# Optimization experiments

Measured on AMD Instinct MI355X. Metric: run time of the kernel, lower is better.

The kernel has to match this reference:

```python
import jax, jax.numpy as jnp
import numpy as np

D_MODEL = 2048
N_HEADS = 16
HEAD_DIM = D_MODEL // N_HEADS
D_FF = 4 * D_MODEL
B, L = 2, 2048
EPS = 1e-5


def _layernorm(x, g, b):
    mu = jnp.mean(x, axis=-1, keepdims=True)
    var = jnp.var(x, axis=-1, keepdims=True)
    return (x - mu) * jax.lax.rsqrt(var + EPS) * g + b


def setup_inputs() -> dict:
    key = jax.random.key(0)
    ks = jax.random.split(key, 8)
    s = 0.02
    x = jax.random.normal(ks[0], (B, L, D_MODEL), dtype=jnp.float32)
    # causal 4-D float mask [B,1,L,L]: 1 = attend, 0 = masked
    attention_mask = jnp.broadcast_to(
        jnp.tril(jnp.ones((L, L), dtype=jnp.float32))[None, None], (B, 1, L, L)
    )
    w_qkv = jax.random.normal(ks[1], (D_MODEL, 3 * D_MODEL), dtype=jnp.float32) * s
    w_o = jax.random.normal(ks[2], (D_MODEL, D_MODEL), dtype=jnp.float32) * s
    w1 = jax.random.normal(ks[3], (D_MODEL, D_FF), dtype=jnp.float32) * s
    b1 = jnp.zeros((D_FF,), dtype=jnp.float32)
    w2 = jax.random.normal(ks[4], (D_FF, D_MODEL), dtype=jnp.float32) * s
    b2 = jnp.zeros((D_MODEL,), dtype=jnp.float32)
    g_ln1 = jnp.ones((D_MODEL,), dtype=jnp.float32)
    b_ln1 = jnp.zeros((D_MODEL,), dtype=jnp.float32)
    g_ln2 = jnp.ones((D_MODEL,), dtype=jnp.float32)
    b_ln2 = jnp.zeros((D_MODEL,), dtype=jnp.float32)
    return {
        "x": x, "attention_mask": attention_mask,
        "w_qkv": w_qkv, "w_o": w_o,
        "g_ln1": g_ln1, "b_ln1": b_ln1, "g_ln2": g_ln2, "b_ln2": b_ln2,
        "w1": w1, "b1": b1, "w2": w2, "b2": b2,
    }


def reference(x, attention_mask, w_qkv, w_o, g_ln1, b_ln1, g_ln2, b_ln2, w1, b1, w2, b2):
    Bx, Lx, D = x.shape
    residual = x
    h = _layernorm(x, g_ln1, b_ln1)
    qkv = (h @ w_qkv).reshape(Bx, Lx, 3, N_HEADS, HEAD_DIM)
    q, k, v = jnp.moveaxis(qkv, 2, 0)           # each [B, L, H, Hd]
    q = q.transpose(0, 2, 1, 3)                  # [B, H, L, Hd]
    k = k.transpose(0, 2, 1, 3)
    v = v.transpose(0, 2, 1, 3)
    scores = jnp.einsum("bhqd,bhkd->bhqk", q, k) / np.float32(np.sqrt(HEAD_DIM))
    scores = scores + (1.0 - attention_mask) * -10000.0  # 4-D float mask branch
    attn = jax.nn.softmax(scores, axis=-1)
    out = jnp.einsum("bhqk,bhkd->bhqd", attn, v)
    out = out.transpose(0, 2, 1, 3).reshape(Bx, Lx, D)
    out = out @ w_o
    x2 = residual + out
    h2 = _layernorm(x2, g_ln2, b_ln2)
    mlp = jax.nn.gelu(h2 @ w1 + b1, approximate=False) @ w2 + b2
    return x2 + mlp
```

## Files before the change

### kernel.cpp

```cpp
#include <hip/hip_runtime.h>
#include <hip/hip_bf16.h>

#define DM   2048
#define LSEQ 2048
#define NB   2
#define NH   16
#define HDIM 128
#define DFF  8192

typedef __attribute__((ext_vector_type(8))) short bf16x8;
typedef __attribute__((ext_vector_type(4))) float f32x4;

typedef __attribute__((address_space(1))) void gvoid;
typedef __attribute__((address_space(3))) void lvoid;
#define GLDS16(g, s) __builtin_amdgcn_global_load_lds((const gvoid*)(g), (lvoid*)(s), 16, 0, 0)

__device__ __forceinline__ unsigned short f2b(float f) {
    __hip_bfloat16 h = __float2bfloat16(f);
    return *reinterpret_cast<unsigned short*>(&h);
}

__global__ __launch_bounds__(256) void transpose_bf16(const float* __restrict__ in,
                                                      unsigned short* __restrict__ out,
                                                      int R, int C) {
    __shared__ float t[32][33];
    const int c0 = blockIdx.x * 32, r0 = blockIdx.y * 32;
    const int tx = threadIdx.x, ty = threadIdx.y;
#pragma unroll
    for (int i = 0; i < 4; i++)
        t[ty + 8 * i][tx] = in[(size_t)(r0 + ty + 8 * i) * C + c0 + tx];
    __syncthreads();
#pragma unroll
    for (int i = 0; i < 4; i++)
        out[(size_t)(c0 + ty + 8 * i) * R + r0 + tx] = f2b(t[tx][ty + 8 * i]);
}

__global__ __launch_bounds__(256) void ln_k(const float* __restrict__ x,
                                            const float* __restrict__ g,
                                            const float* __restrict__ bta,
                                            unsigned short* __restrict__ out) {
    const int row = blockIdx.x, tid = threadIdx.x;
    const float* xr = x + (size_t)row * DM;
    float4 v0 = *(const float4*)&xr[tid * 4];
    float4 v1 = *(const float4*)&xr[1024 + tid * 4];
    float s  = v0.x + v0.y + v0.z + v0.w + v1.x + v1.y + v1.z + v1.w;
    float ss = v0.x * v0.x + v0.y * v0.y + v0.z * v0.z + v0.w * v0.w
             + v1.x * v1.x + v1.y * v1.y + v1.z * v1.z + v1.w * v1.w;
#pragma unroll
    for (int o = 32; o; o >>= 1) { s += __shfl_down(s, o); ss += __shfl_down(ss, o); }
    __shared__ float red[8];
    const int w = tid >> 6, l = tid & 63;
    if (l == 0) { red[w] = s; red[4 + w] = ss; }
    __syncthreads();
    s  = red[0] + red[1] + red[2] + red[3];
    ss = red[4] + red[5] + red[6] + red[7];
    const float mu  = s * (1.0f / DM);
    const float var = ss * (1.0f / DM) - mu * mu;
    const float rst = rsqrtf(var + 1e-5f);
    float4 g0 = *(const float4*)&g[tid * 4];
    float4 b0 = *(const float4*)&bta[tid * 4];
    float4 g1 = *(const float4*)&g[1024 + tid * 4];
    float4 b1 = *(const float4*)&bta[1024 + tid * 4];
    ushort4 o0, o1;
    o0.x = f2b((v0.x - mu) * rst * g0.x + b0.x);
    o0.y = f2b((v0.y - mu) * rst * g0.y + b0.y);
    o0.z = f2b((v0.z - mu) * rst * g0.z + b0.z);
    o0.w = f2b((v0.w - mu) * rst * g0.w + b0.w);
    o1.x = f2b((v1.x - mu) * rst * g1.x + b1.x);
    o1.y = f2b((v1.y - mu) * rst * g1.y + b1.y);
    o1.z = f2b((v1.z - mu) * rst * g1.z + b1.z);
    o1.w = f2b((v1.w - mu) * rst * g1.w + b1.w);
    *(ushort4*)&out[(size_t)row * DM + tid * 4] = o0;
    *(ushort4*)&out[(size_t)row * DM + 1024 + tid * 4] = o1;
}

template <bool BIAS, bool GELU_, bool RES, bool OUTBF>
__global__ __launch_bounds__(256) void gemm_k(const unsigned short* __restrict__ A,
                                              const unsigned short* __restrict__ Bt,
                                              const float* __restrict__ bias,
                                              const float* __restrict__ res,
                                              void* __restrict__ outp,
                                              int M, int N, int K) {
    __shared__ unsigned short Al[128 * 32];
    __shared__ unsigned short Bl[128 * 32];
    const int tid = threadIdx.x, w = tid >> 6, l = tid & 63;
    const int n0 = blockIdx.x * 128, m0 = blockIdx.y * 128;
    const int wr = (w >> 1) * 64, wc = (w & 1) * 64;
    const int lr = l & 15, ko = (l >> 4) * 8;
    f32x4 acc[4][4] = {};

    const int srow = w * 32 + (l >> 2);
    const int skk  = (l & 3) * 8;
    const unsigned short* ga0 = A + (size_t)(m0 + srow) * K + skk;
    const unsigned short* ga1 = ga0 + (size_t)16 * K;
    const unsigned short* gb0 = Bt + (size_t)(n0 + srow) * K + skk;
    const unsigned short* gb1 = gb0 + (size_t)16 * K;
    unsigned short* la = &Al[w * 1024];
    unsigned short* lb = &Bl[w * 1024];
    const int nk = K >> 5;
    for (int kt = 0; kt < nk; ++kt) {
        GLDS16(ga0, la);
        GLDS16(ga1, la + 512);
        GLDS16(gb0, lb);
        GLDS16(gb1, lb + 512);
        ga0 += 32; ga1 += 32; gb0 += 32; gb1 += 32;
        __syncthreads();
        bf16x8 af[4], bv[4];
#pragma unroll
        for (int i = 0; i < 4; i++) af[i] = *(const bf16x8*)&Al[(wr + i * 16 + lr) * 32 + ko];
#pragma unroll
        for (int i = 0; i < 4; i++) bv[i] = *(const bf16x8*)&Bl[(wc + i * 16 + lr) * 32 + ko];
#pragma unroll
        for (int i = 0; i < 4; i++)
#pragma unroll
            for (int j = 0; j < 4; j++)
                acc[i][j] = __builtin_amdgcn_mfma_f32_16x16x32_bf16(af[i], bv[j], acc[i][j], 0, 0, 0);
        __syncthreads();
    }
#pragma unroll
    for (int j = 0; j < 4; j++) {
        const int col = n0 + wc + j * 16 + lr;
        const float bvv = BIAS ? bias[col] : 0.0f;
#pragma unroll
        for (int i = 0; i < 4; i++) {
#pragma unroll
            for (int r = 0; r < 4; r++) {
                const int row = m0 + wr + i * 16 + (l >> 4) * 4 + r;
                float v = acc[i][j][r] + bvv;
                if (GELU_) v = 0.5f * v * (1.0f + erff(v * 0.7071067811865476f));
                if (RES) v += res[(size_t)row * N + col];
                if (OUTBF) ((unsigned short*)outp)[(size_t)row * N + col] = f2b(v);
                else       ((float*)outp)[(size_t)row * N + col] = v;
            }
        }
    }
}

__global__ __launch_bounds__(256) void flash_attn_k(const unsigned short* __restrict__ qkv,
                                                    unsigned short* __restrict__ out) {
    __shared__ unsigned short Kl[64 * 136];
    __shared__ unsigned short Vt[128 * 64];
    __shared__ unsigned short Pl[4][16 * 72];
    const int tid = threadIdx.x, w = tid >> 6, l = tid & 63;
    const int bh = blockIdx.y, b = bh >> 4, h = bh & 15;
    const int lr = l & 15, lg = l >> 4;
    const float sc = 0.08838834764831845f;
    const int NT = LSEQ / 64;

#pragma unroll 1
    for (int pi = 0; pi < 2; ++pi) {
        const int qt = (pi == 0) ? (int)blockIdx.x : (NT - 1 - (int)blockIdx.x);
        const int qw = qt * 64 + w * 16;

        bf16x8 qf[4];
        {
            const unsigned short* qb = qkv + (size_t)(b * LSEQ + qw + lr) * (3 * DM) + h * HDIM + lg * 8;
#pragma unroll
            for (int kc = 0; kc < 4; kc++) qf[kc] = *(const bf16x8*)(qb + kc * 32);
        }
        f32x4 O[8] = {};
        float m_run[4] = {-1e30f, -1e30f, -1e30f, -1e30f};
        float l_run[4] = {};

        for (int kt = 0; kt <= qt; ++kt) {
            const int k0 = kt * 64;
#pragma unroll
            for (int i = 0; i < 4; i++) {
                const int seg = i * 256 + tid;
                const int row = seg >> 4;
                const int c8  = (seg & 15) * 8;
                const unsigned short* src = qkv + (size_t)(b * LSEQ + k0 + row) * (3 * DM) + DM + h * HDIM + c8;
                *(uint4*)&Kl[row * 136 + c8] = *(const uint4*)src;
                unsigned short tmp[8];
                *(uint4*)tmp = *(const uint4*)(src + DM);
#pragma unroll
                for (int j = 0; j < 8; j++) {
                    const int d = c8 + j;
                    Vt[d * 64 + (row ^ ((((d >> 3) ^ d) & 7) << 3))] = tmp[j];
                }
            }
            __syncthreads();
            f32x4 S[4] = {};
#pragma unroll
            for (int st = 0; st < 4; ++st)
#pragma unroll
                for (int kc = 0; kc < 4; kc++) {
                    bf16x8 kb = *(const bf16x8*)&Kl[(st * 16 + lr) * 136 + kc * 32 + lg * 8];
                    S[st] = __builtin_amdgcn_mfma_f32_16x16x32_bf16(qf[kc], kb, S[st], 0, 0, 0);
                }
            const bool last = (kt == qt);
#pragma unroll
            for (int r = 0; r < 4; r++) {
                const int row = qw + lg * 4 + r;
                float s0 = S[0][r] * sc, s1 = S[1][r] * sc, s2 = S[2][r] * sc, s3 = S[3][r] * sc;
                if (last) {
                    if (k0 +  0 + lr > row) s0 = -1e30f;
                    if (k0 + 16 + lr > row) s1 = -1e30f;
                    if (k0 + 32 + lr > row) s2 = -1e30f;
                    if (k0 + 48 + lr > row) s3 = -1e30f;
                }
                float mt = fmaxf(fmaxf(s0, s1), fmaxf(s2, s3));
                mt = fmaxf(mt, __shfl_xor(mt, 1));
                mt = fmaxf(mt, __shfl_xor(mt, 2));
                mt = fmaxf(mt, __shfl_xor(mt, 4));
                mt = fmaxf(mt, __shfl_xor(mt, 8));
                const float mn = fmaxf(m_run[r], mt);
                const float al = __expf(m_run[r] - mn);
                m_run[r] = mn;
                float p0 = __expf(s0 - mn), p1 = __expf(s1 - mn), p2 = __expf(s2 - mn), p3 = __expf(s3 - mn);
                float ts = p0 + p1 + p2 + p3;
                ts += __shfl_xor(ts, 1);
                ts += __shfl_xor(ts, 2);
                ts += __shfl_xor(ts, 4);
                ts += __shfl_xor(ts, 8);
                l_run[r] = l_run[r] * al + ts;
#pragma unroll
                for (int c = 0; c < 8; c++) O[c][r] *= al;
                unsigned short* pr = &Pl[w][(lg * 4 + r) * 72 + lr];
                pr[0] = f2b(p0); pr[16] = f2b(p1); pr[32] = f2b(p2); pr[48] = f2b(p3);
            }
#pragma unroll
            for (int ks = 0; ks < 2; ++ks) {
                bf16x8 pa = *(const bf16x8*)&Pl[w][lr * 72 + ks * 32 + lg * 8];
#pragma unroll
                for (int c = 0; c < 8; c++) {
                    const int d = c * 16 + lr;
                    bf16x8 vb = *(const bf16x8*)&Vt[d * 64 + ((ks * 32 + lg * 8) ^ ((((d >> 3) ^ d) & 7) << 3))];
                    O[c] = __builtin_amdgcn_mfma_f32_16x16x32_bf16(pa, vb, O[c], 0, 0, 0);
                }
            }
            __syncthreads();
        }
#pragma unroll
        for (int r = 0; r < 4; r++) {
            const float inv = 1.0f / l_run[r];
            const size_t ro = (size_t)(b * LSEQ + qw + lg * 4 + r) * DM + h * HDIM;
#pragma unroll
            for (int c = 0; c < 8; c++) out[ro + c * 16 + lr] = f2b(O[c][r] * inv);
        }
    }
}

extern "C" void kernel_launch(void* const* d_in, const int* in_sizes, int n_in,
                              void* d_out, int out_size, void* d_ws, size_t ws_size,
                              hipStream_t stream) {
    const float* x     = (const float*)d_in[0];
    const float* w_qkv = (const float*)d_in[2];
    const float* w_o   = (const float*)d_in[3];
    const float* g1    = (const float*)d_in[4];
    const float* bl1   = (const float*)d_in[5];
    const float* g2    = (const float*)d_in[6];
    const float* bl2   = (const float*)d_in[7];
    const float* w1    = (const float*)d_in[8];
    const float* b1    = (const float*)d_in[9];
    const float* w2    = (const float*)d_in[10];
    const float* b2    = (const float*)d_in[11];
    float* out = (float*)d_out;

    unsigned char* p = (unsigned char*)d_ws;
    unsigned short* wqkvT = (unsigned short*)p; p += (size_t)3 * DM * DM * 2;
    unsigned short* woT   = (unsigned short*)p; p += (size_t)DM * DM * 2;
    unsigned short* w1T   = (unsigned short*)p; p += (size_t)DFF * DM * 2;
    unsigned short* w2T   = (unsigned short*)p; p += (size_t)DM * DFF * 2;
    unsigned short* hbuf  = (unsigned short*)p; p += (size_t)NB * LSEQ * DM * 2;
    unsigned short* big   = (unsigned short*)p; p += (size_t)NB * LSEQ * DFF * 2;
    float* x2 = out;

    const int R = NB * LSEQ;
    dim3 tb(32, 8);
    transpose_bf16<<<dim3(3 * DM / 32, DM / 32), tb, 0, stream>>>(w_qkv, wqkvT, DM, 3 * DM);
    transpose_bf16<<<dim3(DM / 32, DM / 32), tb, 0, stream>>>(w_o, woT, DM, DM);
    transpose_bf16<<<dim3(DFF / 32, DM / 32), tb, 0, stream>>>(w1, w1T, DM, DFF);
    transpose_bf16<<<dim3(DM / 32, DFF / 32), tb, 0, stream>>>(w2, w2T, DFF, DM);

    ln_k<<<R, 256, 0, stream>>>(x, g1, bl1, hbuf);
    gemm_k<false, false, false, true><<<dim3(3 * DM / 128, R / 128), 256, 0, stream>>>(
        hbuf, wqkvT, nullptr, nullptr, big, R, 3 * DM, DM);
    flash_attn_k<<<dim3(LSEQ / 128, NB * NH), 256, 0, stream>>>(big, hbuf);
    gemm_k<false, false, true, false><<<dim3(DM / 128, R / 128), 256, 0, stream>>>(
        hbuf, woT, nullptr, x, x2, R, DM, DM);
    ln_k<<<R, 256, 0, stream>>>(x2, g2, bl2, hbuf);
    gemm_k<true, true, false, true><<<dim3(DFF / 128, R / 128), 256, 0, stream>>>(
        hbuf, w1T, b1, nullptr, big, R, DFF, DM);
    gemm_k<true, false, true, false><<<dim3(DM / 128, R / 128), 256, 0, stream>>>(
        big, w2T, b2, x2, out, R, DM, DFF);
}
```

Measured before the change: 805.9 us.

## Add 256x256 eight-wave pipelined GEMM for QKV and FFN1 projections

```diff
diff --git a/kernel.cpp b/kernel.cpp
--- a/kernel.cpp
+++ b/kernel.cpp
@@ -136,6 +136,158 @@
     }
 }
 
+#define WAITVM4() asm volatile("s_waitcnt vmcnt(4)" ::: "memory")
+#define WAITVM0() asm volatile("s_waitcnt vmcnt(0)" ::: "memory")
+#define WAITLG()  asm volatile("s_waitcnt lgkmcnt(0)" ::: "memory")
+#define MFMA_BEGIN() do { __builtin_amdgcn_s_barrier(); WAITLG(); \
+    __builtin_amdgcn_sched_barrier(0); __builtin_amdgcn_s_setprio(1); } while (0)
+#define MFMA_END() do { __builtin_amdgcn_s_setprio(0); __builtin_amdgcn_s_barrier(); } while (0)
+
+template <int S, int HM>
+__device__ __forceinline__ void read_a(const unsigned short* LDSu, bf16x8 (&af)[8],
+                                       int wr, int lr, int ko) {
+    const unsigned short* pa = LDSu + S * 16384 + wr * 8192;
+#pragma unroll
+    for (int mi = 0; mi < 4; mi++)
+#pragma unroll
+        for (int ks = 0; ks < 2; ks++)
+            af[mi * 2 + ks] = *(const bf16x8*)&pa[ks * 4096 + (HM * 64 + mi * 16 + lr) * 32 + ko];
+}
+template <int S, int HN>
+__device__ __forceinline__ void read_b(const unsigned short* LDSu, bf16x8 (&bf)[4],
+                                       int wc, int lr, int ko) {
+    const unsigned short* pb = LDSu + 32768 + S * 16384 + (wc >> 1) * 8192;
+#pragma unroll
+    for (int nj = 0; nj < 2; nj++)
+#pragma unroll
+        for (int ks = 0; ks < 2; ks++)
+            bf[nj * 2 + ks] = *(const bf16x8*)&pb[ks * 4096 + ((wc & 1) * 64 + HN * 32 + nj * 16 + lr) * 32 + ko];
+}
+template <int HM, int HN>
+__device__ __forceinline__ void quad(f32x4 (&acc)[8][4], const bf16x8 (&af)[8],
+                                     const bf16x8 (&bf)[4]) {
+#pragma unroll
+    for (int mi = 0; mi < 4; mi++)
+#pragma unroll
+        for (int nj = 0; nj < 2; nj++)
+#pragma unroll
+            for (int ks = 0; ks < 2; ks++)
+                acc[HM * 4 + mi][HN * 2 + nj] = __builtin_amdgcn_mfma_f32_16x16x32_bf16(
+                    af[mi * 2 + ks], bf[nj * 2 + ks], acc[HM * 4 + mi][HN * 2 + nj], 0, 0, 0);
+}
+
+template <bool BIAS, bool GELU_>
+__global__ __launch_bounds__(512, 2) void gemm8_k(const unsigned short* __restrict__ A,
+                                                  const unsigned short* __restrict__ Bt,
+                                                  const float* __restrict__ bias,
+                                                  unsigned short* __restrict__ out,
+                                                  int N, int K, int nbx) {
+    extern __shared__ unsigned short LDSu[];
+    const int tid = threadIdx.x, w = tid >> 6, l = tid & 63;
+    const int wr = w >> 2, wc = w & 3;
+    const int lr = l & 15, lg = l >> 4, ko = lg * 8;
+    const int id = blockIdx.x, nwg = gridDim.x;
+    const int swz = (id & 7) * (nwg >> 3) + (id >> 3);
+    const int m0 = (swz / nbx) * 256, n0 = (swz % nbx) * 256;
+
+    const int r = tid >> 2, cc0 = (tid & 3) * 8;
+    const unsigned short* a0row = A + (size_t)(m0 + r) * K + cc0;
+    const unsigned short* a1row = a0row + (size_t)128 * K;
+    const unsigned short* b0row = Bt + (size_t)(n0 + r) * K + cc0;
+    const unsigned short* b1row = b0row + (size_t)128 * K;
+
+#define STAGE_A(S, H, ROW, KOFF) do { \
+    GLDS16((ROW) + (KOFF),      LDSu + (S) * 16384 + (H) * 8192 + tid * 8); \
+    GLDS16((ROW) + (KOFF) + 32, LDSu + (S) * 16384 + (H) * 8192 + 4096 + tid * 8); } while (0)
+#define STAGE_B(S, H, ROW, KOFF) do { \
+    GLDS16((ROW) + (KOFF),      LDSu + 32768 + (S) * 16384 + (H) * 8192 + tid * 8); \
+    GLDS16((ROW) + (KOFF) + 32, LDSu + 32768 + (S) * 16384 + (H) * 8192 + 4096 + tid * 8); } while (0)
+
+    f32x4 acc[8][4] = {};
+    bf16x8 af[8], bf0[4], bf1[4];
+
+    STAGE_A(0, 0, a0row, 0);
+    STAGE_A(0, 1, a1row, 0);
+    STAGE_B(0, 0, b0row, 0);
+    STAGE_B(0, 1, b1row, 0);
+    STAGE_B(1, 0, b0row, 64);
+    STAGE_B(1, 1, b1row, 64);
+    WAITVM4();
+    __builtin_amdgcn_s_barrier();
+
+    const int niter = K >> 7;
+    for (int i = 0; i < niter; ++i) {
+        const bool last = (i == niter - 1);
+        const int k1 = (2 * i + 1) * 64, k2 = k1 + 64, k3 = k1 + 128;
+        read_a<0, 0>(LDSu, af, wr, lr, ko);
+        read_b<0, 0>(LDSu, bf0, wc, lr, ko);
+        STAGE_A(1, 0, a0row, k1);
+        MFMA_BEGIN(); quad<0, 0>(acc, af, bf0); MFMA_END();
+        read_b<0, 1>(LDSu, bf1, wc, lr, ko);
+        STAGE_A(1, 1, a1row, k1);
+        MFMA_BEGIN(); quad<0, 1>(acc, af, bf1); MFMA_END();
+        read_a<0, 1>(LDSu, af, wr, lr, ko);
+        if (!last) STAGE_B(0, 0, b0row, k2);
+        MFMA_BEGIN(); quad<1, 1>(acc, af, bf1); MFMA_END();
+        if (!last) { STAGE_B(0, 1, b1row, k2); WAITVM4(); } else { WAITVM0(); }
+        MFMA_BEGIN(); quad<1, 0>(acc, af, bf0); MFMA_END();
+        read_a<1, 0>(LDSu, af, wr, lr, ko);
+        read_b<1, 0>(LDSu, bf0, wc, lr, ko);
+        if (!last) STAGE_A(0, 0, a0row, k2);
+        MFMA_BEGIN(); quad<0, 0>(acc, af, bf0); MFMA_END();
+        read_b<1, 1>(LDSu, bf1, wc, lr, ko);
+        if (!last) STAGE_A(0, 1, a1row, k2);
+        MFMA_BEGIN(); quad<0, 1>(acc, af, bf1); MFMA_END();
+        read_a<1, 1>(LDSu, af, wr, lr, ko);
+        if (!last) STAGE_B(1, 0, b0row, k3);
+        MFMA_BEGIN(); quad<1, 1>(acc, af, bf1); MFMA_END();
+        if (!last) { STAGE_B(1, 1, b1row, k3); WAITVM4(); }
+        MFMA_BEGIN(); quad<1, 0>(acc, af, bf0); MFMA_END();
+    }
+
+    float* eb = (float*)&LDSu[(size_t)w * 2176];
+    const int row16 = l >> 2, ch = l & 3;
+    float4 bv[4];
+    if (BIAS) {
+#pragma unroll
+        for (int q = 0; q < 4; q++)
+            bv[q] = *(const float4*)&bias[n0 + wc * 64 + ch * 16 + q * 4];
+    }
+#pragma unroll 1
+    for (int mi8 = 0; mi8 < 8; ++mi8) {
+        WAITLG();
+        __builtin_amdgcn_sched_barrier(0);
+#pragma unroll
+        for (int nj = 0; nj < 4; nj++)
+#pragma unroll
+            for (int rr = 0; rr < 4; rr++)
+                eb[(lg * 4 + rr) * 68 + nj * 16 + lr] = acc[mi8][nj][rr];
+        WAITLG();
+        __builtin_amdgcn_sched_barrier(0);
+        alignas(16) unsigned short tmp[16];
+#pragma unroll
+        for (int q = 0; q < 4; q++) {
+            float4 v = *(const float4*)&eb[row16 * 68 + ch * 16 + q * 4];
+            float e0 = v.x, e1 = v.y, e2 = v.z, e3 = v.w;
+            if (BIAS) { e0 += bv[q].x; e1 += bv[q].y; e2 += bv[q].z; e3 += bv[q].w; }
+            if (GELU_) {
+                e0 = 0.5f * e0 * (1.0f + erff(e0 * 0.7071067811865476f));
+                e1 = 0.5f * e1 * (1.0f + erff(e1 * 0.7071067811865476f));
+                e2 = 0.5f * e2 * (1.0f + erff(e2 * 0.7071067811865476f));
+                e3 = 0.5f * e3 * (1.0f + erff(e3 * 0.7071067811865476f));
+            }
+            tmp[q * 4 + 0] = f2b(e0); tmp[q * 4 + 1] = f2b(e1);
+            tmp[q * 4 + 2] = f2b(e2); tmp[q * 4 + 3] = f2b(e3);
+        }
+        unsigned short* dst = out + (size_t)(m0 + wr * 128 + mi8 * 16 + row16) * N
+                              + n0 + wc * 64 + ch * 16;
+        *(uint4*)dst = *(const uint4*)tmp;
+        *(uint4*)(dst + 8) = *(const uint4*)(tmp + 8);
+    }
+#undef STAGE_A
+#undef STAGE_B
+}
+
 __global__ __launch_bounds__(256) void flash_attn_k(const unsigned short* __restrict__ qkv,
                                                     unsigned short* __restrict__ out) {
     __shared__ unsigned short Kl[64 * 136];
@@ -188,12 +340,12 @@
                     bf16x8 kb = *(const bf16x8*)&Kl[(st * 16 + lr) * 136 + kc * 32 + lg * 8];
                     S[st] = __builtin_amdgcn_mfma_f32_16x16x32_bf16(qf[kc], kb, S[st], 0, 0, 0);
                 }
-            const bool last = (kt == qt);
-#pragma unroll
-            for (int r = 0; r < 4; r++) {
-                const int row = qw + lg * 4 + r;
-                float s0 = S[0][r] * sc, s1 = S[1][r] * sc, s2 = S[2][r] * sc, s3 = S[3][r] * sc;
-                if (last) {
+            const bool lastt = (kt == qt);
+#pragma unroll
+            for (int rq = 0; rq < 4; rq++) {
+                const int row = qw + lg * 4 + rq;
+                float s0 = S[0][rq] * sc, s1 = S[1][rq] * sc, s2 = S[2][rq] * sc, s3 = S[3][rq] * sc;
+                if (lastt) {
                     if (k0 +  0 + lr > row) s0 = -1e30f;
                     if (k0 + 16 + lr > row) s1 = -1e30f;
                     if (k0 + 32 + lr > row) s2 = -1e30f;
@@ -204,19 +356,19 @@
                 mt = fmaxf(mt, __shfl_xor(mt, 2));
                 mt = fmaxf(mt, __shfl_xor(mt, 4));
                 mt = fmaxf(mt, __shfl_xor(mt, 8));
-                const float mn = fmaxf(m_run[r], mt);
-                const float al = __expf(m_run[r] - mn);
-                m_run[r] = mn;
+                const float mn = fmaxf(m_run[rq], mt);
+                const float al = __expf(m_run[rq] - mn);
+                m_run[rq] = mn;
                 float p0 = __expf(s0 - mn), p1 = __expf(s1 - mn), p2 = __expf(s2 - mn), p3 = __expf(s3 - mn);
                 float ts = p0 + p1 + p2 + p3;
                 ts += __shfl_xor(ts, 1);
                 ts += __shfl_xor(ts, 2);
                 ts += __shfl_xor(ts, 4);
                 ts += __shfl_xor(ts, 8);
-                l_run[r] = l_run[r] * al + ts;
-#pragma unroll
-                for (int c = 0; c < 8; c++) O[c][r] *= al;
-                unsigned short* pr = &Pl[w][(lg * 4 + r) * 72 + lr];
+                l_run[rq] = l_run[rq] * al + ts;
+#pragma unroll
+                for (int c = 0; c < 8; c++) O[c][rq] *= al;
+                unsigned short* pr = &Pl[w][(lg * 4 + rq) * 72 + lr];
                 pr[0] = f2b(p0); pr[16] = f2b(p1); pr[32] = f2b(p2); pr[48] = f2b(p3);
             }
 #pragma unroll
@@ -232,11 +384,11 @@
             __syncthreads();
         }
 #pragma unroll
-        for (int r = 0; r < 4; r++) {
-            const float inv = 1.0f / l_run[r];
-            const size_t ro = (size_t)(b * LSEQ + qw + lg * 4 + r) * DM + h * HDIM;
-#pragma unroll
-            for (int c = 0; c < 8; c++) out[ro + c * 16 + lr] = f2b(O[c][r] * inv);
+        for (int rq = 0; rq < 4; rq++) {
+            const float inv = 1.0f / l_run[rq];
+            const size_t ro = (size_t)(b * LSEQ + qw + lg * 4 + rq) * DM + h * HDIM;
+#pragma unroll
+            for (int c = 0; c < 8; c++) out[ro + c * 16 + lr] = f2b(O[c][rq] * inv);
         }
     }
 }
@@ -274,14 +426,14 @@
     transpose_bf16<<<dim3(DM / 32, DFF / 32), tb, 0, stream>>>(w2, w2T, DFF, DM);
 
     ln_k<<<R, 256, 0, stream>>>(x, g1, bl1, hbuf);
-    gemm_k<false, false, false, true><<<dim3(3 * DM / 128, R / 128), 256, 0, stream>>>(
-        hbuf, wqkvT, nullptr, nullptr, big, R, 3 * DM, DM);
+    gemm8_k<false, false><<<(R / 256) * (3 * DM / 256), 512, 131072, stream>>>(
+        hbuf, wqkvT, nullptr, big, 3 * DM, DM, 3 * DM / 256);
     flash_attn_k<<<dim3(LSEQ / 128, NB * NH), 256, 0, stream>>>(big, hbuf);
     gemm_k<false, false, true, false><<<dim3(DM / 128, R / 128), 256, 0, stream>>>(
         hbuf, woT, nullptr, x, x2, R, DM, DM);
     ln_k<<<R, 256, 0, stream>>>(x2, g2, bl2, hbuf);
-    gemm_k<true, true, false, true><<<dim3(DFF / 128, R / 128), 256, 0, stream>>>(
-        hbuf, w1T, b1, nullptr, big, R, DFF, DM);
+    gemm8_k<true, true><<<(R / 256) * (DFF / 256), 512, 131072, stream>>>(
+        hbuf, w1T, b1, big, DFF, DM, DFF / 256);
     gemm_k<true, false, true, false><<<dim3(DM / 128, R / 128), 256, 0, stream>>>(
         big, w2T, b2, x2, out, R, DM, DFF);
 }
```

Result: slower. 905.4 us (+12.3%).

## Stage bf16 GEMM epilogue through LDS for vectorized stores and remap block order

Applied to the files above, without the earlier changes.

```diff
diff --git a/kernel.cpp b/kernel.cpp
--- a/kernel.cpp
+++ b/kernel.cpp
@@ -14,6 +14,7 @@
 typedef __attribute__((address_space(1))) void gvoid;
 typedef __attribute__((address_space(3))) void lvoid;
 #define GLDS16(g, s) __builtin_amdgcn_global_load_lds((const gvoid*)(g), (lvoid*)(s), 16, 0, 0)
+#define WAITLG()  asm volatile("s_waitcnt lgkmcnt(0)" ::: "memory")
 
 __device__ __forceinline__ unsigned short f2b(float f) {
     __hip_bfloat16 h = __float2bfloat16(f);
@@ -75,18 +76,23 @@
 }
 
 template <bool BIAS, bool GELU_, bool RES, bool OUTBF>
-__global__ __launch_bounds__(256) void gemm_k(const unsigned short* __restrict__ A,
-                                              const unsigned short* __restrict__ Bt,
-                                              const float* __restrict__ bias,
-                                              const float* __restrict__ res,
-                                              void* __restrict__ outp,
-                                              int M, int N, int K) {
-    __shared__ unsigned short Al[128 * 32];
-    __shared__ unsigned short Bl[128 * 32];
+__global__ __launch_bounds__(256) void gemm2_k(const unsigned short* __restrict__ A,
+                                               const unsigned short* __restrict__ Bt,
+                                               const float* __restrict__ bias,
+                                               const float* __restrict__ res,
+                                               void* __restrict__ outp,
+                                               int M, int N, int K) {
+    __shared__ unsigned short SH[8704];
+    unsigned short* Al = SH;
+    unsigned short* Bl = SH + 4096;
     const int tid = threadIdx.x, w = tid >> 6, l = tid & 63;
-    const int n0 = blockIdx.x * 128, m0 = blockIdx.y * 128;
+    const int flat = blockIdx.y * gridDim.x + blockIdx.x;
+    const int xx = flat & 7, jj = flat >> 3;
+    const int by = 4 * xx + (jj & 3);
+    const int bx = jj >> 2;
+    const int n0 = bx * 128, m0 = by * 128;
     const int wr = (w >> 1) * 64, wc = (w & 1) * 64;
-    const int lr = l & 15, ko = (l >> 4) * 8;
+    const int lr = l & 15, lg = l >> 4, ko = lg * 8;
     f32x4 acc[4][4] = {};
 
     const int srow = w * 32 + (l >> 2);
@@ -117,20 +123,61 @@
                 acc[i][j] = __builtin_amdgcn_mfma_f32_16x16x32_bf16(af[i], bv[j], acc[i][j], 0, 0, 0);
         __syncthreads();
     }
-#pragma unroll
-    for (int j = 0; j < 4; j++) {
-        const int col = n0 + wc + j * 16 + lr;
-        const float bvv = BIAS ? bias[col] : 0.0f;
+    if (OUTBF) {
+        float* eb = (float*)SH + w * 1088;
+        const int row16 = l >> 2, ch = l & 3;
+        float4 bvv[4];
+        if (BIAS) {
+#pragma unroll
+            for (int q = 0; q < 4; q++)
+                bvv[q] = *(const float4*)&bias[n0 + wc + ch * 16 + q * 4];
+        }
 #pragma unroll
         for (int i = 0; i < 4; i++) {
-#pragma unroll
-            for (int r = 0; r < 4; r++) {
-                const int row = m0 + wr + i * 16 + (l >> 4) * 4 + r;
-                float v = acc[i][j][r] + bvv;
-                if (GELU_) v = 0.5f * v * (1.0f + erff(v * 0.7071067811865476f));
-                if (RES) v += res[(size_t)row * N + col];
-                if (OUTBF) ((unsigned short*)outp)[(size_t)row * N + col] = f2b(v);
-                else       ((float*)outp)[(size_t)row * N + col] = v;
+            WAITLG();
+            __builtin_amdgcn_sched_barrier(0);
+#pragma unroll
+            for (int j = 0; j < 4; j++)
+#pragma unroll
+                for (int r = 0; r < 4; r++)
+                    eb[(lg * 4 + r) * 68 + j * 16 + lr] = acc[i][j][r];
+            WAITLG();
+            __builtin_amdgcn_sched_barrier(0);
+            alignas(16) unsigned short tmp[16];
+#pragma unroll
+            for (int q = 0; q < 4; q++) {
+                float4 v = *(const float4*)&eb[row16 * 68 + ch * 16 + q * 4];
+                float e0 = v.x, e1 = v.y, e2 = v.z, e3 = v.w;
+                if (BIAS) { e0 += bvv[q].x; e1 += bvv[q].y; e2 += bvv[q].z; e3 += bvv[q].w; }
+                if (GELU_) {
+                    e0 = 0.5f * e0 * (1.0f + erff(e0 * 0.7071067811865476f));
+                    e1 = 0.5f * e1 * (1.0f + erff(e1 * 0.7071067811865476f));
+                    e2 = 0.5f * e2 * (1.0f + erff(e2 * 0.7071067811865476f));
+                    e3 = 0.5f * e3 * (1.0f + erff(e3 * 0.7071067811865476f));
+                }
+                tmp[q * 4 + 0] = f2b(e0); tmp[q * 4 + 1] = f2b(e1);
+                tmp[q * 4 + 2] = f2b(e2); tmp[q * 4 + 3] = f2b(e3);
+            }
+            unsigned short* dst = (unsigned short*)outp
+                                  + (size_t)(m0 + wr + i * 16 + row16) * N + n0 + wc + ch * 16;
+            *(uint4*)dst = *(const uint4*)tmp;
+            *(uint4*)(dst + 8) = *(const uint4*)(tmp + 8);
+        }
+    } else {
+#pragma unroll
+        for (int j = 0; j < 4; j++) {
+            const int col = n0 + wc + j * 16 + lr;
+            const float bvv = BIAS ? bias[col] : 0.0f;
+#pragma unroll
+            for (int i = 0; i < 4; i++) {
+#pragma unroll
+                for (int r = 0; r < 4; r++) {
+                    const int row = m0 + wr + i * 16 + lg * 4 + r;
+                    float v = acc[i][j][r] + bvv;
+                    if (GELU_) v = 0.5f * v * (1.0f + erff(v * 0.7071067811865476f));
+                    if (RES) v += res[(size_t)row * N + col];
+                    ((float*)outp)[(size_t)row * N + col] = v;
+                }
             }
         }
     }
@@ -188,12 +235,12 @@
                     bf16x8 kb = *(const bf16x8*)&Kl[(st * 16 + lr) * 136 + kc * 32 + lg * 8];
                     S[st] = __builtin_amdgcn_mfma_f32_16x16x32_bf16(qf[kc], kb, S[st], 0, 0, 0);
                 }
-            const bool last = (kt == qt);
-#pragma unroll
-            for (int r = 0; r < 4; r++) {
-                const int row = qw + lg * 4 + r;
-                float s0 = S[0][r] * sc, s1 = S[1][r] * sc, s2 = S[2][r] * sc, s3 = S[3][r] * sc;
-                if (last) {
+            const bool lastt = (kt == qt);
+#pragma unroll
+            for (int rq = 0; rq < 4; rq++) {
+                const int row = qw + lg * 4 + rq;
+                float s0 = S[0][rq] * sc, s1 = S[1][rq] * sc, s2 = S[2][rq] * sc, s3 = S[3][rq] * sc;
+                if (lastt) {
                     if (k0 +  0 + lr > row) s0 = -1e30f;
                     if (k0 + 16 + lr > row) s1 = -1e30f;
                     if (k0 + 32 + lr > row) s2 = -1e30f;
@@ -204,19 +251,19 @@
                 mt = fmaxf(mt, __shfl_xor(mt, 2));
                 mt = fmaxf(mt, __shfl_xor(mt, 4));
                 mt = fmaxf(mt, __shfl_xor(mt, 8));
-                const float mn = fmaxf(m_run[r], mt);
-                const float al = __expf(m_run[r] - mn);
-                m_run[r] = mn;
+                const float mn = fmaxf(m_run[rq], mt);
+                const float al = __expf(m_run[rq] - mn);
+                m_run[rq] = mn;
                 float p0 = __expf(s0 - mn), p1 = __expf(s1 - mn), p2 = __expf(s2 - mn), p3 = __expf(s3 - mn);
                 float ts = p0 + p1 + p2 + p3;
                 ts += __shfl_xor(ts, 1);
                 ts += __shfl_xor(ts, 2);
                 ts += __shfl_xor(ts, 4);
                 ts += __shfl_xor(ts, 8);
-                l_run[r] = l_run[r] * al + ts;
-#pragma unroll
-                for (int c = 0; c < 8; c++) O[c][r] *= al;
-                unsigned short* pr = &Pl[w][(lg * 4 + r) * 72 + lr];
+                l_run[rq] = l_run[rq] * al + ts;
+#pragma unroll
+                for (int c = 0; c < 8; c++) O[c][rq] *= al;
+                unsigned short* pr = &Pl[w][(lg * 4 + rq) * 72 + lr];
                 pr[0] = f2b(p0); pr[16] = f2b(p1); pr[32] = f2b(p2); pr[48] = f2b(p3);
             }
 #pragma unroll
@@ -232,11 +279,11 @@
             __syncthreads();
         }
 #pragma unroll
-        for (int r = 0; r < 4; r++) {
-            const float inv = 1.0f / l_run[r];
-            const size_t ro = (size_t)(b * LSEQ + qw + lg * 4 + r) * DM + h * HDIM;
-#pragma unroll
-            for (int c = 0; c < 8; c++) out[ro + c * 16 + lr] = f2b(O[c][r] * inv);
+        for (int rq = 0; rq < 4; rq++) {
+            const float inv = 1.0f / l_run[rq];
+            const size_t ro = (size_t)(b * LSEQ + qw + lg * 4 + rq) * DM + h * HDIM;
+#pragma unroll
+            for (int c = 0; c < 8; c++) out[ro + c * 16 + lr] = f2b(O[c][rq] * inv);
         }
     }
 }
@@ -274,14 +321,14 @@
     transpose_bf16<<<dim3(DM / 32, DFF / 32), tb, 0, stream>>>(w2, w2T, DFF, DM);
 
     ln_k<<<R, 256, 0, stream>>>(x, g1, bl1, hbuf);
-    gemm_k<false, false, false, true><<<dim3(3 * DM / 128, R / 128), 256, 0, stream>>>(
+    gemm2_k<false, false, false, true><<<dim3(3 * DM / 128, R / 128), 256, 0, stream>>>(
         hbuf, wqkvT, nullptr, nullptr, big, R, 3 * DM, DM);
     flash_attn_k<<<dim3(LSEQ / 128, NB * NH), 256, 0, stream>>>(big, hbuf);
-    gemm_k<false, false, true, false><<<dim3(DM / 128, R / 128), 256, 0, stream>>>(
+    gemm2_k<false, false, true, false><<<dim3(DM / 128, R / 128), 256, 0, stream>>>(
         hbuf, woT, nullptr, x, x2, R, DM, DM);
     ln_k<<<R, 256, 0, stream>>>(x2, g2, bl2, hbuf);
-    gemm_k<true, true, false, true><<<dim3(DFF / 128, R / 128), 256, 0, stream>>>(
+    gemm2_k<true, true, false, true><<<dim3(DFF / 128, R / 128), 256, 0, stream>>>(
         hbuf, w1T, b1, nullptr, big, R, DFF, DM);
-    gemm_k<true, false, true, false><<<dim3(DM / 128, R / 128), 256, 0, stream>>>(
+    gemm2_k<true, false, true, false><<<dim3(DM / 128, R / 128), 256, 0, stream>>>(
         big, w2T, b2, x2, out, R, DM, DFF);
 }
```

Result: no change. 813.5 us (+0.9%).
